# Kernel tuning notes

Hardware: AMD Instinct MI355X
Metric: run time of the kernel (lower is better)

Reference implementation:

```python
import jax, jax.numpy as jnp
import numpy as np

# Symmetric per-tensor int8 fake-quant (dynamic scale), the math that the
# q/k/v/smax matmul-act hooks and the matmul-error hooks apply in QAT mode.
# (With the module's default nn.Identity() hooks this reduces to identity;
# here we model the quantized path the module is designed for.)
QMAX = 127.0

def fake_quant(x):
    s = jnp.max(jnp.abs(x)) / QMAX + 1e-8
    return jnp.clip(jnp.round(x / s), -QMAX, QMAX) * s


def setup_inputs() -> dict:
    key = jax.random.key(0)
    ks = jax.random.split(key, 6)
    T, B, D = 2048, 2, 1024
    std = 0.02
    return {
        "x": jax.random.normal(ks[0], (T, B, D), dtype=jnp.float32),
        "wq": jax.random.normal(ks[1], (D, D), dtype=jnp.float32) * std,
        "bq": jnp.zeros((D,), dtype=jnp.float32),
        "wk": jax.random.normal(ks[2], (D, D), dtype=jnp.float32) * std,
        "bk": jnp.zeros((D,), dtype=jnp.float32),
        "wv": jax.random.normal(ks[3], (D, D), dtype=jnp.float32) * std,
        "bv": jnp.zeros((D,), dtype=jnp.float32),
        "wo": jax.random.normal(ks[4], (D, D), dtype=jnp.float32) * std,
        "bo": jnp.zeros((D,), dtype=jnp.float32),
        "num_heads": 16,
    }


def reference(x, wq, bq, wk, bk, wv, bv, wo, bo, num_heads):
    # x: (T, B, D)  -- fairseq Time x Batch x Channel layout
    T, B, D = x.shape
    H = num_heads
    Dh = D // H
    scaling = Dh ** -0.5

    q = (x @ wq.T + bq) * scaling          # (T, B, D)
    k = x @ wk.T + bk
    v = x @ wv.T + bv

    # view(T, B*H, Dh).transpose(0,1) -> (B*H, T, Dh)
    q = q.reshape(T, B * H, Dh).transpose(1, 0, 2)
    k = k.reshape(T, B * H, Dh).transpose(1, 0, 2)
    v = v.reshape(T, B * H, Dh).transpose(1, 0, 2)

    # attn_weights = k_q_err_quant( bmm(q_act_quant(q), k_act_quant(k)^T) )
    scores = fake_quant(jnp.einsum('bqd,bkd->bqk', fake_quant(q), fake_quant(k)))
    probs = jax.nn.softmax(scores, axis=-1)  # dropout p=0.0

    # attn = smax_v_err_quant( bmm(smax_act_quant(probs), v_act_quant(v)) )
    attn = fake_quant(jnp.einsum('bqk,bkd->bqd', fake_quant(probs), fake_quant(v)))

    attn = attn.transpose(1, 0, 2).reshape(T, B, D)  # back to (T, B, D)
    out = attn @ wo.T + bo
    return out
```

## Files before the change

### kernel.cpp

```cpp
#include <hip/hip_runtime.h>
#include <stdint.h>

#define T_DIM 2048
#define B_DIM 2
#define D_DIM 1024
#define H_DIM 16
#define DH    64
#define G_DIM 32
#define N_ROWS 4096
#define K_DIM 1024

typedef __bf16 bf16x8 __attribute__((ext_vector_type(8)));
typedef float  f32x4  __attribute__((ext_vector_type(4)));
typedef int    i32x4  __attribute__((ext_vector_type(4)));

typedef const __attribute__((address_space(1))) unsigned int* gas_u32;
typedef __attribute__((address_space(3))) unsigned int* las_u32;

static __device__ __forceinline__ void gload16(const void* gsrc, void* ldst) {
  __builtin_amdgcn_global_load_lds((gas_u32)gsrc, (las_u32)ldst, 16, 0, 0);
}

static __device__ __forceinline__ unsigned short f32_to_bf16_rne(float f) {
  unsigned u = __float_as_uint(f);
  u += 0x7FFFu + ((u >> 16) & 1u);
  return (unsigned short)(u >> 16);
}
static __device__ __forceinline__ float bf16_to_f32(unsigned short h) {
  return __uint_as_float(((unsigned)h) << 16);
}

static __device__ __forceinline__ void split4_store(const float* __restrict__ src,
                                                    unsigned short* __restrict__ hi,
                                                    unsigned short* __restrict__ lo,
                                                    size_t i4) {
  float4 x = *reinterpret_cast<const float4*>(src + i4);
  ushort4 h, l;
  { float f = x.x; h.x = f32_to_bf16_rne(f); l.x = f32_to_bf16_rne(f - bf16_to_f32(h.x)); }
  { float f = x.y; h.y = f32_to_bf16_rne(f); l.y = f32_to_bf16_rne(f - bf16_to_f32(h.y)); }
  { float f = x.z; h.z = f32_to_bf16_rne(f); l.z = f32_to_bf16_rne(f - bf16_to_f32(h.z)); }
  { float f = x.w; h.w = f32_to_bf16_rne(f); l.w = f32_to_bf16_rne(f - bf16_to_f32(h.w)); }
  *reinterpret_cast<ushort4*>(hi + i4) = h;
  *reinterpret_cast<ushort4*>(lo + i4) = l;
}

__global__ __launch_bounds__(256) void split_x_kernel(const float* __restrict__ src,
                                                      unsigned short* __restrict__ hi,
                                                      unsigned short* __restrict__ lo) {
  size_t i4 = ((size_t)blockIdx.x * 256 + threadIdx.x) * 4;
  split4_store(src, hi, lo, i4);
}

__global__ __launch_bounds__(256) void split_w_kernel(const float* __restrict__ w0,
                                                      const float* __restrict__ w1,
                                                      const float* __restrict__ w2,
                                                      const float* __restrict__ w3,
                                                      unsigned short* __restrict__ hi,
                                                      unsigned short* __restrict__ lo) {
  const int z = blockIdx.z;
  const float* src = (z == 0) ? w0 : (z == 1) ? w1 : (z == 2) ? w2 : w3;
  size_t base = (size_t)z * (D_DIM * D_DIM);
  size_t i4 = ((size_t)blockIdx.x * 256 + threadIdx.x) * 4;
  split4_store(src, hi + base, lo + base, i4);
}

__global__ __launch_bounds__(256, 2) void gemm_bf16x3_v3(
    const unsigned short* __restrict__ Ahi, const unsigned short* __restrict__ Alo,
    const unsigned short* __restrict__ Whi, const unsigned short* __restrict__ Wlo,
    const float* __restrict__ b0, const float* __restrict__ b1, const float* __restrict__ b2,
    float* __restrict__ C, int ncols, unsigned* __restrict__ scal_base, float alpha0) {
  __shared__ __align__(16) unsigned short sAh[128 * 64];
  __shared__ __align__(16) unsigned short sAl[128 * 64];
  __shared__ __align__(16) unsigned short sWh[128 * 64];
  __shared__ __align__(16) unsigned short sWl[128 * 64];
  __shared__ unsigned sam;
  const int lane = threadIdx.x & 63, wave = threadIdx.x >> 6;
  const int ntn = ncols >> 7;
  const int cpx = gridDim.x >> 3;
  const int bid = blockIdx.x;
  const int swz = (bid & 7) * cpx + (bid >> 3);
  const int tm = swz / ntn, tn = swz - tm * ntn;
  const int rowBase = tm * 128, colBase = tn * 128;
  const int wr = wave >> 1, wc = wave & 1;
  const int lr = lane >> 3, lk = (lane & 7) * 8;
  const int lo = lane & 15, hi4 = lane >> 4;

  f32x4 acc[4][4];
#pragma unroll
  for (int i = 0; i < 4; ++i)
#pragma unroll
    for (int j = 0; j < 4; ++j) acc[i][j] = f32x4{0.f, 0.f, 0.f, 0.f};

  for (int k0 = 0; k0 < K_DIM; k0 += 64) {
    __syncthreads();
#pragma unroll
    for (int i = 0; i < 4; ++i) {
      const int ca = wave * 4 + i;
      const size_t go = (size_t)(rowBase + ca * 8 + lr) * K_DIM + k0 + lk;
      gload16(Ahi + go, &sAh[ca * 512]);
      gload16(Alo + go, &sAl[ca * 512]);
      const size_t gw = (size_t)(colBase + ca * 8 + lr) * K_DIM + k0 + lk;
      gload16(Whi + gw, &sWh[ca * 512]);
      gload16(Wlo + gw, &sWl[ca * 512]);
    }
    __syncthreads();
#pragma unroll
    for (int kk = 0; kk < 64; kk += 32) {
      bf16x8 ah[4], al[4], wh[4], wl[4];
#pragma unroll
      for (int rt = 0; rt < 4; ++rt) {
        const int offA = (wr * 64 + rt * 16 + lo) * 64 + kk + hi4 * 8;
        ah[rt] = *reinterpret_cast<const bf16x8*>(&sAh[offA]);
        al[rt] = *reinterpret_cast<const bf16x8*>(&sAl[offA]);
        const int offW = (wc * 64 + rt * 16 + lo) * 64 + kk + hi4 * 8;
        wh[rt] = *reinterpret_cast<const bf16x8*>(&sWh[offW]);
        wl[rt] = *reinterpret_cast<const bf16x8*>(&sWl[offW]);
      }
#pragma unroll
      for (int jt = 0; jt < 4; ++jt)
#pragma unroll
        for (int rt = 0; rt < 4; ++rt)
          acc[rt][jt] = __builtin_amdgcn_mfma_f32_16x16x32_bf16(ah[rt], wh[jt], acc[rt][jt], 0, 0, 0);
#pragma unroll
      for (int jt = 0; jt < 4; ++jt)
#pragma unroll
        for (int rt = 0; rt < 4; ++rt)
          acc[rt][jt] = __builtin_amdgcn_mfma_f32_16x16x32_bf16(ah[rt], wl[jt], acc[rt][jt], 0, 0, 0);
#pragma unroll
      for (int jt = 0; jt < 4; ++jt)
#pragma unroll
        for (int rt = 0; rt < 4; ++rt)
          acc[rt][jt] = __builtin_amdgcn_mfma_f32_16x16x32_bf16(al[rt], wh[jt], acc[rt][jt], 0, 0, 0);
    }
  }
  const int sec = colBase >> 10;
  const float* bp = (sec == 0) ? b0 : ((sec == 1) ? b1 : b2);
  const float alpha = (sec == 0) ? alpha0 : 1.0f;
  const int colL = (colBase & 1023) + wc * 64;
  float bj[4];
#pragma unroll
  for (int jt = 0; jt < 4; ++jt) bj[jt] = bp[colL + jt * 16 + lo];
  float am = 0.f;
#pragma unroll
  for (int rt = 0; rt < 4; ++rt)
#pragma unroll
    for (int jt = 0; jt < 4; ++jt)
#pragma unroll
      for (int r = 0; r < 4; ++r) {
        float v = (acc[rt][jt][r] + bj[jt]) * alpha;
        C[(size_t)(rowBase + wr * 64 + rt * 16 + hi4 * 4 + r) * ncols + colBase + wc * 64 +
          jt * 16 + lo] = v;
        am = fmaxf(am, fabsf(v));
      }
#pragma unroll
  for (int s = 32; s; s >>= 1) am = fmaxf(am, __shfl_xor(am, s));
  if (threadIdx.x == 0) sam = 0u;
  __syncthreads();
  if (lane == 0) atomicMax(&sam, __float_as_uint(am));
  __syncthreads();
  if (threadIdx.x == 0) atomicMax(scal_base + sec, sam);
}

__global__ __launch_bounds__(256) void quant_qk_kernel(const float* __restrict__ qkv32,
                                                       signed char* __restrict__ qi8,
                                                       signed char* __restrict__ ki8,
                                                       unsigned* __restrict__ scal) {
  if (blockIdx.x == 0 && blockIdx.y == 0 && threadIdx.x == 0) scal[4] = 0x7F800000u;
  const int which = blockIdx.y;
  signed char* dst = which ? ki8 : qi8;
  const float s = __uint_as_float(scal[which]) / 127.0f + 1e-8f;
  size_t i4 = ((size_t)blockIdx.x * 256 + threadIdx.x) * 4;
  int d = (int)(i4 & (D_DIM - 1));
  int row = (int)(i4 >> 10);
  float4 x = *reinterpret_cast<const float4*>(qkv32 + (size_t)row * 3072 + which * 1024 + d);
  int t = row >> 1, b = row & 1;
  int h = d >> 6, dh = d & 63;
  char4 c;
  { float q = rintf(x.x / s); q = fminf(127.f, fmaxf(-127.f, q)); c.x = (signed char)q; }
  { float q = rintf(x.y / s); q = fminf(127.f, fmaxf(-127.f, q)); c.y = (signed char)q; }
  { float q = rintf(x.z / s); q = fminf(127.f, fmaxf(-127.f, q)); c.z = (signed char)q; }
  { float q = rintf(x.w / s); q = fminf(127.f, fmaxf(-127.f, q)); c.w = (signed char)q; }
  *reinterpret_cast<char4*>(dst + (((size_t)(b * H_DIM + h) * T_DIM + t) * DH + dh)) = c;
}

__global__ __launch_bounds__(256) void quant_v_kernel(const float* __restrict__ qkv32,
                                                      signed char* __restrict__ viT8,
                                                      const unsigned* __restrict__ scal) {
  const float s = __uint_as_float(scal[2]) / 127.0f + 1e-8f;
  const int g = blockIdx.y, t0 = blockIdx.x * 64;
  const int b = g >> 4, h = g & 15;
  __shared__ signed char tile[64][68];
  const int tid = threadIdx.x;
#pragma unroll
  for (int rep = 0; rep < 4; ++rep) {
    int tl = tid >> 2;
    int f4 = (tid & 3) + rep * 4;
    const float* p = qkv32 + ((size_t)(t0 + tl) * B_DIM + b) * 3072 + 2048 + h * 64 + f4 * 4;
    float4 x = *reinterpret_cast<const float4*>(p);
    char4 c;
    { float q = rintf(x.x / s); q = fminf(127.f, fmaxf(-127.f, q)); c.x = (signed char)q; }
    { float q = rintf(x.y / s); q = fminf(127.f, fmaxf(-127.f, q)); c.y = (signed char)q; }
    { float q = rintf(x.z / s); q = fminf(127.f, fmaxf(-127.f, q)); c.z = (signed char)q; }
    { float q = rintf(x.w / s); q = fminf(127.f, fmaxf(-127.f, q)); c.w = (signed char)q; }
    *reinterpret_cast<char4*>(&tile[tl][f4 * 4]) = c;
  }
  __syncthreads();
  const int dh = tid >> 2, tq = tid & 3;
  signed char outb[16];
#pragma unroll
  for (int j = 0; j < 16; ++j) outb[j] = tile[tq * 16 + j][dh];
  i32x4 vv;
  __builtin_memcpy(&vv, outb, 16);
  *reinterpret_cast<i32x4*>(viT8 + ((size_t)g * DH + dh) * T_DIM + t0 + tq * 16) = vv;
}

static __device__ __forceinline__ void xpose4(int h, int& p0, int& p1, int& p2, int& p3) {
  const bool b0 = (h & 1), b1 = (h & 2);
  int s0 = __shfl_xor(p0, 16), s1 = __shfl_xor(p1, 16);
  int s2 = __shfl_xor(p2, 16), s3 = __shfl_xor(p3, 16);
  int q0 = b0 ? s1 : p0;
  int q1 = b0 ? p1 : s0;
  int q2 = b0 ? s3 : p2;
  int q3 = b0 ? p3 : s2;
  int u0 = __shfl_xor(q0, 32), u1 = __shfl_xor(q1, 32);
  int u2 = __shfl_xor(q2, 32), u3 = __shfl_xor(q3, 32);
  p0 = b1 ? u2 : q0;
  p1 = b1 ? u3 : q1;
  p2 = b1 ? q2 : u0;
  p3 = b1 ? q3 : u1;
}

__global__ __launch_bounds__(256) void attn_smax_kernel(const signed char* __restrict__ qi8,
                                                        const signed char* __restrict__ ki8,
                                                        unsigned* __restrict__ scal) {
  const int lane = threadIdx.x & 63, wave = threadIdx.x >> 6;
  const int g = blockIdx.y;
  const int qb = blockIdx.x * 64 + wave * 16;
  const int lo = lane & 15, hi4 = lane >> 4;
  const signed char* qg = qi8 + (size_t)g * T_DIM * DH;
  const signed char* kg = ki8 + (size_t)g * T_DIM * DH;
  const i32x4 qfr = *reinterpret_cast<const i32x4*>(qg + (size_t)(qb + lo) * DH + hi4 * 16);
  const i32x4 zero = {0, 0, 0, 0};
  int mx = -2147483647, mn = 2147483647;
#pragma unroll 4
  for (int kc = 0; kc < T_DIM; kc += 16) {
    i32x4 kfr = *reinterpret_cast<const i32x4*>(kg + (size_t)(kc + lo) * DH + hi4 * 16);
    i32x4 sc = __builtin_amdgcn_mfma_i32_16x16x64_i8(kfr, qfr, zero, 0, 0, 0);
#pragma unroll
    for (int r = 0; r < 4; ++r) { mx = sc[r] > mx ? sc[r] : mx; mn = sc[r] < mn ? sc[r] : mn; }
  }
  int am = mx > -mn ? mx : -mn;
#pragma unroll
  for (int s = 32; s; s >>= 1) { int o = __shfl_xor(am, s); am = o > am ? o : am; }
  __shared__ int sm;
  if (threadIdx.x == 0) sm = 0;
  __syncthreads();
  if (lane == 0) atomicMax(&sm, am);
  __syncthreads();
  if (threadIdx.x == 0) atomicMax((int*)&scal[3], sm);
}

__global__ __launch_bounds__(256) void attn_stats_kernel(const signed char* __restrict__ qi8,
                                                         const signed char* __restrict__ ki8,
                                                         unsigned* __restrict__ scal,
                                                         float* __restrict__ rowZ,
                                                         float* __restrict__ rowL) {
  const float sq = __uint_as_float(scal[0]) / 127.0f + 1e-8f;
  const float sk = __uint_as_float(scal[1]) / 127.0f + 1e-8f;
  const float sqsk = sq * sk;
  const float smax = sqsk * (float)(int)scal[3];
  const float s_s = smax / 127.0f + 1e-8f;
  const float ratio = sqsk / s_s;
  const float a = s_s * 1.4426950408889634f;
  const float c = -127.0f * a;
  __shared__ float gLut[256];
  const int tid = threadIdx.x;
  if (tid < 255) gLut[tid] = exp2f(fmaf((float)(tid - 127), a, c));
  __syncthreads();
  const int lane = tid & 63, wave = tid >> 6;
  const int g = blockIdx.y;
  const int qb = blockIdx.x * 64 + wave * 16;
  const int lo = lane & 15, hi4 = lane >> 4;
  const signed char* qg = qi8 + (size_t)g * T_DIM * DH;
  const signed char* kg = ki8 + (size_t)g * T_DIM * DH;
  const i32x4 qfr = *reinterpret_cast<const i32x4*>(qg + (size_t)(qb + lo) * DH + hi4 * 16);
  const i32x4 zero = {0, 0, 0, 0};
  int scmax = -2147483647;
  float zp = 0.f;
#pragma unroll 4
  for (int kc = 0; kc < T_DIM; kc += 16) {
    i32x4 kfr = *reinterpret_cast<const i32x4*>(kg + (size_t)(kc + lo) * DH + hi4 * 16);
    i32x4 sc = __builtin_amdgcn_mfma_i32_16x16x64_i8(kfr, qfr, zero, 0, 0, 0);
#pragma unroll
    for (int r = 0; r < 4; ++r) {
      scmax = sc[r] > scmax ? sc[r] : scmax;
      int idx = (int)rintf((float)sc[r] * ratio) + 127;
      zp += gLut[idx];
    }
  }
  { int o = __shfl_xor(scmax, 16); scmax = o > scmax ? o : scmax; }
  zp += __shfl_xor(zp, 16);
  { int o = __shfl_xor(scmax, 32); scmax = o > scmax ? o : scmax; }
  zp += __shfl_xor(zp, 32);
  float mx = rintf((float)scmax * ratio);
  float Z = zp * exp2f((127.0f - mx) * a);
  if (hi4 == 0) {
    rowZ[(size_t)g * T_DIM + qb + lo] = Z;
    rowL[(size_t)g * T_DIM + qb + lo] = mx;
  }
  float zm = Z;
#pragma unroll
  for (int s = 32; s; s >>= 1) zm = fminf(zm, __shfl_xor(zm, s));
  __shared__ unsigned szm;
  if (tid == 0) szm = 0x7F800000u;
  __syncthreads();
  if (lane == 0) atomicMin(&szm, __float_as_uint(zm));
  __syncthreads();
  if (tid == 0) atomicMin(&scal[4], szm);
}

#define LUTS 260
__global__ __launch_bounds__(256) void attn_pv_kernel(const signed char* __restrict__ qi8,
                                                      const signed char* __restrict__ ki8,
                                                      const signed char* __restrict__ viT8,
                                                      const float* __restrict__ rowZ,
                                                      const float* __restrict__ rowL,
                                                      unsigned* __restrict__ scal,
                                                      int* __restrict__ attn_out) {
  const float sq = __uint_as_float(scal[0]) / 127.0f + 1e-8f;
  const float sk = __uint_as_float(scal[1]) / 127.0f + 1e-8f;
  const float sqsk = sq * sk;
  const float smax = sqsk * (float)(int)scal[3];
  const float s_s = smax / 127.0f + 1e-8f;
  const float ratio = sqsk / s_s;
  const float a = s_s * 1.4426950408889634f;
  const float maxp = 1.0f / __uint_as_float(scal[4]);
  const float s_p = maxp / 127.0f + 1e-8f;
  const float inv_sp = 1.0f / s_p;
  const int tid = threadIdx.x;
  const int lane = tid & 63, wave = tid >> 6;
  const int g = blockIdx.y;
  const int qb0 = blockIdx.x * 64;
  const int qb = qb0 + wave * 16;
  const int lo = lane & 15, hi4 = lane >> 4;

  __shared__ signed char plut[64 * LUTS];
  for (int n = tid; n < 64 * 256; n += 256) {
    const int row = n >> 8, i = n & 255;
    if (i < 255) {
      const float Zr = rowZ[(size_t)g * T_DIM + qb0 + row];
      const float lm = rowL[(size_t)g * T_DIM + qb0 + row];
      const float crow = (1.0f / Zr) * inv_sp;
      const float bneg = -lm * a;
      const float lf = (float)(i - 127);
      const float e = exp2f(fmaf(lf, a, bneg));
      const float pf = fminf(rintf(e * crow), 127.f);
      plut[row * LUTS + i] = (signed char)(int)pf;
    }
  }
  __syncthreads();

  const signed char* qg = qi8 + (size_t)g * T_DIM * DH;
  const signed char* kg = ki8 + (size_t)g * T_DIM * DH;
  const signed char* vg = viT8 + (size_t)g * DH * T_DIM;
  const i32x4 qfr = *reinterpret_cast<const i32x4*>(qg + (size_t)(qb + lo) * DH + hi4 * 16);
  const int lbase = (wave * 16 + lo) * LUTS + 127;
  const i32x4 zero = {0, 0, 0, 0};
  i32x4 accv[4];
#pragma unroll
  for (int dt = 0; dt < 4; ++dt) accv[dt] = zero;

  for (int kc = 0; kc < T_DIM; kc += 64) {
    int pk[4];
#pragma unroll
    for (int t = 0; t < 4; ++t) {
      i32x4 kfr =
          *reinterpret_cast<const i32x4*>(kg + (size_t)(kc + t * 16 + lo) * DH + hi4 * 16);
      i32x4 sc = __builtin_amdgcn_mfma_i32_16x16x64_i8(kfr, qfr, zero, 0, 0, 0);
      unsigned b0, b1, b2, b3;
      { int idx = (int)rintf((float)sc[0] * ratio); b0 = (unsigned char)plut[lbase + idx]; }
      { int idx = (int)rintf((float)sc[1] * ratio); b1 = (unsigned char)plut[lbase + idx]; }
      { int idx = (int)rintf((float)sc[2] * ratio); b2 = (unsigned char)plut[lbase + idx]; }
      { int idx = (int)rintf((float)sc[3] * ratio); b3 = (unsigned char)plut[lbase + idx]; }
      pk[t] = (int)(b0 | (b1 << 8) | (b2 << 16) | (b3 << 24));
    }
    xpose4(hi4, pk[0], pk[1], pk[2], pk[3]);
    const i32x4 pfr = {pk[0], pk[1], pk[2], pk[3]};
#pragma unroll
    for (int dt = 0; dt < 4; ++dt) {
      i32x4 vfr =
          *reinterpret_cast<const i32x4*>(vg + (size_t)(dt * 16 + lo) * T_DIM + kc + hi4 * 16);
      accv[dt] = __builtin_amdgcn_mfma_i32_16x16x64_i8(pfr, vfr, accv[dt], 0, 0, 0);
    }
  }
  int am = 0;
#pragma unroll
  for (int dt = 0; dt < 4; ++dt)
#pragma unroll
    for (int r = 0; r < 4; ++r) {
      int v = accv[dt][r];
      attn_out[((size_t)g * T_DIM + qb + hi4 * 4 + r) * DH + dt * 16 + lo] = v;
      int av = v < 0 ? -v : v;
      am = av > am ? av : am;
    }
#pragma unroll
  for (int s = 32; s; s >>= 1) { int o = __shfl_xor(am, s); am = o > am ? o : am; }
  __shared__ int sm;
  if (tid == 0) sm = 0;
  __syncthreads();
  if (lane == 0) atomicMax(&sm, am);
  __syncthreads();
  if (tid == 0) atomicMax((int*)&scal[5], sm);
}

__global__ __launch_bounds__(256) void quant_attn_kernel(const int* __restrict__ attn_i32,
                                                         unsigned short* __restrict__ aq_hi,
                                                         unsigned short* __restrict__ aq_lo,
                                                         const unsigned* __restrict__ scal) {
  const float sv = __uint_as_float(scal[2]) / 127.0f + 1e-8f;
  const float maxp = 1.0f / __uint_as_float(scal[4]);
  const float s_p = maxp / 127.0f + 1e-8f;
  const float spsv = s_p * sv;
  const float amax = spsv * (float)(int)scal[5];
  const float s_a = amax / 127.0f + 1e-8f;
  size_t i4 = ((size_t)blockIdx.x * 256 + threadIdx.x) * 4;
  i32x4 iv = *reinterpret_cast<const i32x4*>(attn_i32 + i4);
  int dh0 = (int)(i4 & 63);
  int t = (int)((i4 >> 6) & (T_DIM - 1));
  int g = (int)(i4 >> 17);
  int b = g >> 4, h = g & 15;
  ushort4 hh, ll;
  { float v = (float)iv[0] * spsv; float lf = fminf(127.f, fmaxf(-127.f, rintf(v / s_a)));
    float qv = lf * s_a; hh.x = f32_to_bf16_rne(qv); ll.x = f32_to_bf16_rne(qv - bf16_to_f32(hh.x)); }
  { float v = (float)iv[1] * spsv; float lf = fminf(127.f, fmaxf(-127.f, rintf(v / s_a)));
    float qv = lf * s_a; hh.y = f32_to_bf16_rne(qv); ll.y = f32_to_bf16_rne(qv - bf16_to_f32(hh.y)); }
  { float v = (float)iv[2] * spsv; float lf = fminf(127.f, fmaxf(-127.f, rintf(v / s_a)));
    float qv = lf * s_a; hh.z = f32_to_bf16_rne(qv); ll.z = f32_to_bf16_rne(qv - bf16_to_f32(hh.z)); }
  { float v = (float)iv[3] * spsv; float lf = fminf(127.f, fmaxf(-127.f, rintf(v / s_a)));
    float qv = lf * s_a; hh.w = f32_to_bf16_rne(qv); ll.w = f32_to_bf16_rne(qv - bf16_to_f32(hh.w)); }
  size_t o = (size_t)(t * B_DIM + b) * D_DIM + h * 64 + dh0;
  *reinterpret_cast<ushort4*>(aq_hi + o) = hh;
  *reinterpret_cast<ushort4*>(aq_lo + o) = ll;
}

extern "C" void kernel_launch(void* const* d_in, const int* in_sizes, int n_in,
                              void* d_out, int out_size, void* d_ws, size_t ws_size,
                              hipStream_t stream) {
  (void)in_sizes; (void)n_in; (void)out_size;
  const float* x  = (const float*)d_in[0];
  const float* wq = (const float*)d_in[1];
  const float* bq = (const float*)d_in[2];
  const float* wk = (const float*)d_in[3];
  const float* bk = (const float*)d_in[4];
  const float* wv = (const float*)d_in[5];
  const float* bv = (const float*)d_in[6];
  const float* wo = (const float*)d_in[7];
  const float* bo = (const float*)d_in[8];
  float* out = (float*)d_out;
  char* ws = (char*)d_ws;

  constexpr size_t SZ_ROW   = (size_t)G_DIM * T_DIM * 4;
  constexpr size_t SZ_XSPL  = (size_t)N_ROWS * D_DIM * 2;
  constexpr size_t SZ_WSPL  = (size_t)4 * D_DIM * D_DIM * 2;
  constexpr size_t SZ_QKV   = (size_t)N_ROWS * 3072 * 4;
  constexpr size_t SZ_I8    = (size_t)G_DIM * T_DIM * DH;
  constexpr size_t OFF_ROWZ = 256;
  constexpr size_t OFF_ROWL = OFF_ROWZ + SZ_ROW;
  constexpr size_t OFF_XHI  = OFF_ROWL + SZ_ROW;
  constexpr size_t OFF_XLO  = OFF_XHI + SZ_XSPL;
  constexpr size_t OFF_WHI  = OFF_XLO + SZ_XSPL;
  constexpr size_t OFF_WLO  = OFF_WHI + SZ_WSPL;
  constexpr size_t OFF_QKV  = OFF_WLO + SZ_WSPL;
  constexpr size_t OFF_QI8  = OFF_QKV + SZ_QKV;
  constexpr size_t OFF_KI8  = OFF_QI8 + SZ_I8;
  constexpr size_t OFF_VIT8 = OFF_KI8 + SZ_I8;
  constexpr size_t OFF_END  = OFF_VIT8 + SZ_I8;
  if (ws_size < OFF_END) return;

  unsigned* scal = (unsigned*)ws;
  float* rowZ = (float*)(ws + OFF_ROWZ);
  float* rowL = (float*)(ws + OFF_ROWL);
  unsigned short* x_hi = (unsigned short*)(ws + OFF_XHI);
  unsigned short* x_lo = (unsigned short*)(ws + OFF_XLO);
  unsigned short* w_hi = (unsigned short*)(ws + OFF_WHI);
  unsigned short* w_lo = (unsigned short*)(ws + OFF_WLO);
  float* qkv32 = (float*)(ws + OFF_QKV);
  signed char* qi8 = (signed char*)(ws + OFF_QI8);
  signed char* ki8 = (signed char*)(ws + OFF_KI8);
  signed char* viT8 = (signed char*)(ws + OFF_VIT8);
  int* attn_i32 = (int*)(ws + OFF_QKV);
  unsigned short* aq_hi = x_hi;
  unsigned short* aq_lo = x_lo;

  hipMemsetAsync(ws, 0, 64, stream);
  split_x_kernel<<<4096, 256, 0, stream>>>(x, x_hi, x_lo);
  split_w_kernel<<<dim3(1024, 1, 4), 256, 0, stream>>>(wq, wk, wv, wo, w_hi, w_lo);
  gemm_bf16x3_v3<<<768, 256, 0, stream>>>(x_hi, x_lo, w_hi, w_lo, bq, bk, bv, qkv32, 3072,
                                          scal, 0.125f);
  quant_qk_kernel<<<dim3(4096, 2), 256, 0, stream>>>(qkv32, qi8, ki8, scal);
  quant_v_kernel<<<dim3(32, 32), 256, 0, stream>>>(qkv32, viT8, scal);
  attn_smax_kernel<<<dim3(32, 32), 256, 0, stream>>>(qi8, ki8, scal);
  attn_stats_kernel<<<dim3(32, 32), 256, 0, stream>>>(qi8, ki8, scal, rowZ, rowL);
  attn_pv_kernel<<<dim3(32, 32), 256, 0, stream>>>(qi8, ki8, viT8, rowZ, rowL, scal, attn_i32);
  quant_attn_kernel<<<4096, 256, 0, stream>>>(attn_i32, aq_hi, aq_lo, scal);
  gemm_bf16x3_v3<<<256, 256, 0, stream>>>(aq_hi, aq_lo, w_hi + 3145728, w_lo + 3145728, bo, bo,
                                          bo, out, 1024, scal + 6, 1.0f);
}
```

Baseline: 429.7 us.

## Split attention key range across two wave groups and compute probs inline

The three attention kernels now launch 512 threads per block, with two groups of four waves each handling half of the key sequence. Partial max/sum and PV accumulators are combined through shared memory. The per-block probability LUT in the PV kernel is replaced by a direct exp2 evaluation, with rounding done via a float magic-number add. This raises parallelism per block and removes the LUT build, at the cost of more transcendental ops and possible rounding differences, including losing the explicit clamp at 127.

```diff
diff --git a/kernel.cpp b/kernel.cpp
--- a/kernel.cpp
+++ b/kernel.cpp
@@ -230,12 +230,14 @@
   p3 = b1 ? q3 : u1;
 }
 
-__global__ __launch_bounds__(256) void attn_smax_kernel(const signed char* __restrict__ qi8,
-                                                        const signed char* __restrict__ ki8,
-                                                        unsigned* __restrict__ scal) {
-  const int lane = threadIdx.x & 63, wave = threadIdx.x >> 6;
+__global__ __launch_bounds__(512, 8) void attn_smax_kernel(const signed char* __restrict__ qi8,
+                                                           const signed char* __restrict__ ki8,
+                                                           unsigned* __restrict__ scal) {
+  const int tid = threadIdx.x;
+  const int lane = tid & 63, wave = tid >> 6;
   const int g = blockIdx.y;
-  const int qb = blockIdx.x * 64 + wave * 16;
+  const int qb = blockIdx.x * 64 + (wave & 3) * 16;
+  const int k0 = (wave >> 2) * (T_DIM / 2);
   const int lo = lane & 15, hi4 = lane >> 4;
   const signed char* qg = qi8 + (size_t)g * T_DIM * DH;
   const signed char* kg = ki8 + (size_t)g * T_DIM * DH;
@@ -243,7 +245,7 @@
   const i32x4 zero = {0, 0, 0, 0};
   int mx = -2147483647, mn = 2147483647;
 #pragma unroll 4
-  for (int kc = 0; kc < T_DIM; kc += 16) {
+  for (int kc = k0; kc < k0 + T_DIM / 2; kc += 16) {
     i32x4 kfr = *reinterpret_cast<const i32x4*>(kg + (size_t)(kc + lo) * DH + hi4 * 16);
     i32x4 sc = __builtin_amdgcn_mfma_i32_16x16x64_i8(kfr, qfr, zero, 0, 0, 0);
 #pragma unroll
@@ -253,18 +255,18 @@
 #pragma unroll
   for (int s = 32; s; s >>= 1) { int o = __shfl_xor(am, s); am = o > am ? o : am; }
   __shared__ int sm;
-  if (threadIdx.x == 0) sm = 0;
+  if (tid == 0) sm = 0;
   __syncthreads();
   if (lane == 0) atomicMax(&sm, am);
   __syncthreads();
-  if (threadIdx.x == 0) atomicMax((int*)&scal[3], sm);
-}
-
-__global__ __launch_bounds__(256) void attn_stats_kernel(const signed char* __restrict__ qi8,
-                                                         const signed char* __restrict__ ki8,
-                                                         unsigned* __restrict__ scal,
-                                                         float* __restrict__ rowZ,
-                                                         float* __restrict__ rowL) {
+  if (tid == 0) atomicMax((int*)&scal[3], sm);
+}
+
+__global__ __launch_bounds__(512, 8) void attn_stats_kernel(const signed char* __restrict__ qi8,
+                                                            const signed char* __restrict__ ki8,
+                                                            unsigned* __restrict__ scal,
+                                                            float* __restrict__ rowZ,
+                                                            float* __restrict__ rowL) {
   const float sq = __uint_as_float(scal[0]) / 127.0f + 1e-8f;
   const float sk = __uint_as_float(scal[1]) / 127.0f + 1e-8f;
   const float sqsk = sq * sk;
@@ -274,12 +276,17 @@
   const float a = s_s * 1.4426950408889634f;
   const float c = -127.0f * a;
   __shared__ float gLut[256];
+  __shared__ int cmx[4][16];
+  __shared__ float czp[4][16];
+  __shared__ unsigned szm;
   const int tid = threadIdx.x;
   if (tid < 255) gLut[tid] = exp2f(fmaf((float)(tid - 127), a, c));
+  if (tid == 0) szm = 0x7F800000u;
   __syncthreads();
   const int lane = tid & 63, wave = tid >> 6;
   const int g = blockIdx.y;
-  const int qb = blockIdx.x * 64 + wave * 16;
+  const int qb = blockIdx.x * 64 + (wave & 3) * 16;
+  const int k0 = (wave >> 2) * (T_DIM / 2);
   const int lo = lane & 15, hi4 = lane >> 4;
   const signed char* qg = qi8 + (size_t)g * T_DIM * DH;
   const signed char* kg = ki8 + (size_t)g * T_DIM * DH;
@@ -288,7 +295,7 @@
   int scmax = -2147483647;
   float zp = 0.f;
 #pragma unroll 4
-  for (int kc = 0; kc < T_DIM; kc += 16) {
+  for (int kc = k0; kc < k0 + T_DIM / 2; kc += 16) {
     i32x4 kfr = *reinterpret_cast<const i32x4*>(kg + (size_t)(kc + lo) * DH + hi4 * 16);
     i32x4 sc = __builtin_amdgcn_mfma_i32_16x16x64_i8(kfr, qfr, zero, 0, 0, 0);
 #pragma unroll
@@ -302,31 +309,34 @@
   zp += __shfl_xor(zp, 16);
   { int o = __shfl_xor(scmax, 32); scmax = o > scmax ? o : scmax; }
   zp += __shfl_xor(zp, 32);
-  float mx = rintf((float)scmax * ratio);
-  float Z = zp * exp2f((127.0f - mx) * a);
-  if (hi4 == 0) {
-    rowZ[(size_t)g * T_DIM + qb + lo] = Z;
-    rowL[(size_t)g * T_DIM + qb + lo] = mx;
-  }
-  float zm = Z;
-#pragma unroll
-  for (int s = 32; s; s >>= 1) zm = fminf(zm, __shfl_xor(zm, s));
-  __shared__ unsigned szm;
-  if (tid == 0) szm = 0x7F800000u;
-  __syncthreads();
-  if (lane == 0) atomicMin(&szm, __float_as_uint(zm));
+  if (wave >= 4 && hi4 == 0) { cmx[wave - 4][lo] = scmax; czp[wave - 4][lo] = zp; }
+  __syncthreads();
+  if (wave < 4) {
+    int o = cmx[wave][lo];
+    scmax = o > scmax ? o : scmax;
+    zp += czp[wave][lo];
+    float mx = rintf((float)scmax * ratio);
+    float Z = zp * exp2f((127.0f - mx) * a);
+    if (hi4 == 0) {
+      rowZ[(size_t)g * T_DIM + qb + lo] = Z;
+      rowL[(size_t)g * T_DIM + qb + lo] = mx;
+    }
+    float zm = Z;
+#pragma unroll
+    for (int s = 32; s; s >>= 1) zm = fminf(zm, __shfl_xor(zm, s));
+    if (lane == 0) atomicMin(&szm, __float_as_uint(zm));
+  }
   __syncthreads();
   if (tid == 0) atomicMin(&scal[4], szm);
 }
 
-#define LUTS 260
-__global__ __launch_bounds__(256) void attn_pv_kernel(const signed char* __restrict__ qi8,
-                                                      const signed char* __restrict__ ki8,
-                                                      const signed char* __restrict__ viT8,
-                                                      const float* __restrict__ rowZ,
-                                                      const float* __restrict__ rowL,
-                                                      unsigned* __restrict__ scal,
-                                                      int* __restrict__ attn_out) {
+__global__ __launch_bounds__(512, 8) void attn_pv_kernel(const signed char* __restrict__ qi8,
+                                                         const signed char* __restrict__ ki8,
+                                                         const signed char* __restrict__ viT8,
+                                                         const float* __restrict__ rowZ,
+                                                         const float* __restrict__ rowL,
+                                                         unsigned* __restrict__ scal,
+                                                         int* __restrict__ attn_out) {
   const float sq = __uint_as_float(scal[0]) / 127.0f + 1e-8f;
   const float sk = __uint_as_float(scal[1]) / 127.0f + 1e-8f;
   const float sqsk = sq * sk;
@@ -336,53 +346,42 @@
   const float a = s_s * 1.4426950408889634f;
   const float maxp = 1.0f / __uint_as_float(scal[4]);
   const float s_p = maxp / 127.0f + 1e-8f;
-  const float inv_sp = 1.0f / s_p;
   const int tid = threadIdx.x;
   const int lane = tid & 63, wave = tid >> 6;
   const int g = blockIdx.y;
-  const int qb0 = blockIdx.x * 64;
-  const int qb = qb0 + wave * 16;
+  const int qb = blockIdx.x * 64 + (wave & 3) * 16;
+  const int k0 = (wave >> 2) * (T_DIM / 2);
   const int lo = lane & 15, hi4 = lane >> 4;
-
-  __shared__ signed char plut[64 * LUTS];
-  for (int n = tid; n < 64 * 256; n += 256) {
-    const int row = n >> 8, i = n & 255;
-    if (i < 255) {
-      const float Zr = rowZ[(size_t)g * T_DIM + qb0 + row];
-      const float lm = rowL[(size_t)g * T_DIM + qb0 + row];
-      const float crow = (1.0f / Zr) * inv_sp;
-      const float bneg = -lm * a;
-      const float lf = (float)(i - 127);
-      const float e = exp2f(fmaf(lf, a, bneg));
-      const float pf = fminf(rintf(e * crow), 127.f);
-      plut[row * LUTS + i] = (signed char)(int)pf;
-    }
-  }
-  __syncthreads();
 
   const signed char* qg = qi8 + (size_t)g * T_DIM * DH;
   const signed char* kg = ki8 + (size_t)g * T_DIM * DH;
   const signed char* vg = viT8 + (size_t)g * DH * T_DIM;
   const i32x4 qfr = *reinterpret_cast<const i32x4*>(qg + (size_t)(qb + lo) * DH + hi4 * 16);
-  const int lbase = (wave * 16 + lo) * LUTS + 127;
+  const float Zr = rowZ[(size_t)g * T_DIM + qb + lo];
+  const float lm = rowL[(size_t)g * T_DIM + qb + lo];
+  const float bexp = fmaf(-lm, a, -__log2f(Zr * s_p));
   const i32x4 zero = {0, 0, 0, 0};
   i32x4 accv[4];
 #pragma unroll
   for (int dt = 0; dt < 4; ++dt) accv[dt] = zero;
 
-  for (int kc = 0; kc < T_DIM; kc += 64) {
+  for (int kc = k0; kc < k0 + T_DIM / 2; kc += 64) {
     int pk[4];
 #pragma unroll
     for (int t = 0; t < 4; ++t) {
       i32x4 kfr =
           *reinterpret_cast<const i32x4*>(kg + (size_t)(kc + t * 16 + lo) * DH + hi4 * 16);
       i32x4 sc = __builtin_amdgcn_mfma_i32_16x16x64_i8(kfr, qfr, zero, 0, 0, 0);
-      unsigned b0, b1, b2, b3;
-      { int idx = (int)rintf((float)sc[0] * ratio); b0 = (unsigned char)plut[lbase + idx]; }
-      { int idx = (int)rintf((float)sc[1] * ratio); b1 = (unsigned char)plut[lbase + idx]; }
-      { int idx = (int)rintf((float)sc[2] * ratio); b2 = (unsigned char)plut[lbase + idx]; }
-      { int idx = (int)rintf((float)sc[3] * ratio); b3 = (unsigned char)plut[lbase + idx]; }
-      pk[t] = (int)(b0 | (b1 << 8) | (b2 << 16) | (b3 << 24));
+      unsigned u0, u1, u2, u3;
+      { float lf = rintf((float)sc[0] * ratio);
+        u0 = __float_as_uint(exp2f(fmaf(lf, a, bexp)) + 8388608.0f); }
+      { float lf = rintf((float)sc[1] * ratio);
+        u1 = __float_as_uint(exp2f(fmaf(lf, a, bexp)) + 8388608.0f); }
+      { float lf = rintf((float)sc[2] * ratio);
+        u2 = __float_as_uint(exp2f(fmaf(lf, a, bexp)) + 8388608.0f); }
+      { float lf = rintf((float)sc[3] * ratio);
+        u3 = __float_as_uint(exp2f(fmaf(lf, a, bexp)) + 8388608.0f); }
+      pk[t] = (int)((u0 & 255u) | ((u1 & 255u) << 8) | ((u2 & 255u) << 16) | (u3 << 24));
     }
     xpose4(hi4, pk[0], pk[1], pk[2], pk[3]);
     const i32x4 pfr = {pk[0], pk[1], pk[2], pk[3]};
@@ -393,21 +392,30 @@
       accv[dt] = __builtin_amdgcn_mfma_i32_16x16x64_i8(pfr, vfr, accv[dt], 0, 0, 0);
     }
   }
-  int am = 0;
-#pragma unroll
-  for (int dt = 0; dt < 4; ++dt)
-#pragma unroll
-    for (int r = 0; r < 4; ++r) {
-      int v = accv[dt][r];
-      attn_out[((size_t)g * T_DIM + qb + hi4 * 4 + r) * DH + dt * 16 + lo] = v;
-      int av = v < 0 ? -v : v;
-      am = av > am ? av : am;
-    }
-#pragma unroll
-  for (int s = 32; s; s >>= 1) { int o = __shfl_xor(am, s); am = o > am ? o : am; }
+  __shared__ __align__(16) i32x4 cmb[4][64][4];
   __shared__ int sm;
   if (tid == 0) sm = 0;
-  __syncthreads();
+  if (wave >= 4) {
+#pragma unroll
+    for (int dt = 0; dt < 4; ++dt) cmb[wave - 4][lane][dt] = accv[dt];
+  }
+  __syncthreads();
+  int am = 0;
+  if (wave < 4) {
+#pragma unroll
+    for (int dt = 0; dt < 4; ++dt) {
+      i32x4 o = cmb[wave][lane][dt];
+#pragma unroll
+      for (int r = 0; r < 4; ++r) {
+        int v = accv[dt][r] + o[r];
+        attn_out[((size_t)g * T_DIM + qb + hi4 * 4 + r) * DH + dt * 16 + lo] = v;
+        int av = v < 0 ? -v : v;
+        am = av > am ? av : am;
+      }
+    }
+  }
+#pragma unroll
+  for (int s = 32; s; s >>= 1) { int o = __shfl_xor(am, s); am = o > am ? o : am; }
   if (lane == 0) atomicMax(&sm, am);
   __syncthreads();
   if (tid == 0) atomicMax((int*)&scal[5], sm);
@@ -499,9 +507,9 @@
                                           scal, 0.125f);
   quant_qk_kernel<<<dim3(4096, 2), 256, 0, stream>>>(qkv32, qi8, ki8, scal);
   quant_v_kernel<<<dim3(32, 32), 256, 0, stream>>>(qkv32, viT8, scal);
-  attn_smax_kernel<<<dim3(32, 32), 256, 0, stream>>>(qi8, ki8, scal);
-  attn_stats_kernel<<<dim3(32, 32), 256, 0, stream>>>(qi8, ki8, scal, rowZ, rowL);
-  attn_pv_kernel<<<dim3(32, 32), 256, 0, stream>>>(qi8, ki8, viT8, rowZ, rowL, scal, attn_i32);
+  attn_smax_kernel<<<dim3(32, 32), 512, 0, stream>>>(qi8, ki8, scal);
+  attn_stats_kernel<<<dim3(32, 32), 512, 0, stream>>>(qi8, ki8, scal, rowZ, rowL);
+  attn_pv_kernel<<<dim3(32, 32), 512, 0, stream>>>(qi8, ki8, viT8, rowZ, rowL, scal, attn_i32);
   quant_attn_kernel<<<4096, 256, 0, stream>>>(attn_i32, aq_hi, aq_lo, scal);
   gemm_bf16x3_v3<<<256, 256, 0, stream>>>(aq_hi, aq_lo, w_hi + 3145728, w_lo + 3145728, bo, bo,
                                           bo, out, 1024, scal + 6, 1.0f);
```

New measurement: 416.0 us. -3.2%, faster.
